# Kernel tuning notes

Hardware: AMD Instinct MI355X
Metric: run time of the kernel (lower is better)

Reference implementation:

```python
import jax, jax.numpy as jnp
import numpy as np

B, S, D = 4, 4096, 1024
E, C, F = 8, 1024, 2048


def setup_inputs() -> dict:
    key = jax.random.key(0)
    ks = jax.random.split(key, 6)
    # weight init per module: uniform(-bound, bound), bound = sqrt(3)*sqrt(1/3)/sqrt(fan_in) = 1/sqrt(fan_in)
    b_d = 1.0 / np.sqrt(D)
    b_f = 1.0 / np.sqrt(F)
    return {
        "x": jax.random.normal(ks[0], (B, S, D), dtype=jnp.float32),
        "expert_weights": jax.random.uniform(ks[1], (B, E, C), dtype=jnp.float32),
        "token_indices": jax.random.randint(ks[2], (B, E, C), 0, S, dtype=jnp.int64),
        "w1": jax.random.uniform(ks[3], (E, D, F), dtype=jnp.float32, minval=-b_d, maxval=b_d),
        "w2": jax.random.uniform(ks[4], (E, D, F), dtype=jnp.float32, minval=-b_d, maxval=b_d),
        "w3": jax.random.uniform(ks[5], (E, F, D), dtype=jnp.float32, minval=-b_f, maxval=b_f),
    }


def reference(x, expert_weights, token_indices, w1, w2, w3):
    # gather: each expert picks `capacity` tokens from its batch row
    b_idx = jnp.arange(B)[:, None, None]                      # (B,1,1)
    expert_inputs = x[b_idx, token_indices]                   # (B,E,C,D)
    # grouped swiglu FFN per expert (no weight repeat needed: einsum batches over E)
    gate = jax.nn.silu(jnp.einsum('becd,edf->becf', expert_inputs, w1))
    value = jnp.einsum('becd,edf->becf', expert_inputs, w2)
    expert_outputs = jnp.einsum('becf,efd->becd', gate * value, w3)  # (B,E,C,D)
    weighted = expert_outputs * expert_weights[..., None]     # (B,E,C,D)
    # weighted scatter-add combine back to (B,S,D)
    out = jnp.zeros((B, S, D), dtype=x.dtype)
    out = out.at[b_idx, token_indices].add(weighted)
    return out
```

## Files before the change

### kernel.cpp

```cpp
#include <hip/hip_runtime.h>

#define Bn 4
#define Sn 4096
#define Dn 1024
#define En 8
#define Cn 1024
#define Fn 2048
#define Mn (Bn * Cn)

typedef __bf16 bf16x4 __attribute__((ext_vector_type(4)));
typedef __bf16 bf16x8 __attribute__((ext_vector_type(8)));
typedef float f32x4 __attribute__((ext_vector_type(4)));

#define GLOAD16(gsrc, ldst)                                                    \
  __builtin_amdgcn_global_load_lds(                                            \
      (const __attribute__((address_space(1))) void*)(gsrc),                   \
      (__attribute__((address_space(3))) void*)(ldst), 16, 0, 0)

#define VMCNT3() asm volatile("s_waitcnt vmcnt(3)" ::: "memory")
#define VMCNT0() asm volatile("s_waitcnt vmcnt(0)" ::: "memory")
#define SCHEDB() __builtin_amdgcn_sched_barrier(0)
#define SBAR() __builtin_amdgcn_s_barrier()
#define PRIO(p) __builtin_amdgcn_s_setprio(p)

__global__ __launch_bounds__(256) void tcast_kernel(
    const float* __restrict__ in, __bf16* __restrict__ out, int K, int N) {
  __shared__ float t[32][33];
  const int e = blockIdx.z;
  const float* src = in + (size_t)e * K * N;
  __bf16* dst = out + (size_t)e * K * N;
  const int n0 = blockIdx.x << 5, k0 = blockIdx.y << 5;
  const int tx = threadIdx.x & 31, ty = threadIdx.x >> 5;
#pragma unroll
  for (int i = 0; i < 4; ++i)
    t[ty + i * 8][tx] = src[(size_t)(k0 + ty + i * 8) * N + (n0 + tx)];
  __syncthreads();
#pragma unroll
  for (int i = 0; i < 4; ++i)
    dst[(size_t)(n0 + ty + i * 8) * K + (k0 + tx)] = (__bf16)t[tx][ty + i * 8];
}

__global__ __launch_bounds__(256) void gather_cast_kernel(
    const float* __restrict__ x, const int* __restrict__ tok,
    __bf16* __restrict__ Xg) {
  const int gid = blockIdx.x * 4 + (threadIdx.x >> 6);
  const int lane = threadIdx.x & 63;
  const int e = gid >> 12, m = gid & 4095, b = m >> 10, c = m & 1023;
  const int t = tok[((size_t)b * En + e) * Cn + c];
  const float* src = x + ((size_t)b * Sn + t) * Dn;
  __bf16* dst = Xg + (size_t)gid * Dn;
#pragma unroll
  for (int i = 0; i < 4; ++i) {
    f32x4 v = *(const f32x4*)(src + i * 256 + lane * 4);
    bf16x4 o;
    o[0] = (__bf16)v[0];
    o[1] = (__bf16)v[1];
    o[2] = (__bf16)v[2];
    o[3] = (__bf16)v[3];
    *(bf16x4*)(dst + i * 256 + lane * 4) = o;
  }
}


__global__ __launch_bounds__(512, 4) void gemm12_kernel(
    const __bf16* __restrict__ Xg, const float* __restrict__ ew,
    const __bf16* __restrict__ w1T, const __bf16* __restrict__ w2T,
    __bf16* __restrict__ Hbh, int e0) {
  __shared__ __align__(16) char lds[73728];

  const int tid = threadIdx.x;
  const int lane = tid & 63, wid = tid >> 6;
  const int wr = wid >> 2, wc = wid & 3;
  const int mt = blockIdx.x, ft = blockIdx.y, eLoc = blockIdx.z;
  const int e = e0 + eLoc;

  const int srow = tid >> 2;
  const int sof = ((tid & 3) ^ ((tid >> 3) & 3)) << 3;
  const __bf16* pA = Xg + ((size_t)e * Mn + mt * 128 + srow) * Dn + sof;
  const __bf16* pB1 = w1T + ((size_t)e * Fn + ft * 128 + srow) * Dn + sof;
  const __bf16* pB2 = w2T + ((size_t)e * Fn + ft * 128 + srow) * Dn + sof;

  auto stage = [&](int slot) {
    char* d = lds + slot * 24576 + tid * 16;
    GLOAD16(pA, d);
    GLOAD16(pB1, d + 8192);
    GLOAD16(pB2, d + 16384);
    pA += 32;
    pB1 += 32;
    pB2 += 32;
  };

  const int rl = lane & 15, kb = lane >> 4;
  const int swz = (kb ^ ((rl >> 1) & 3)) << 4;

  f32x4 acc[4][4];
  const f32x4 z4 = {0.f, 0.f, 0.f, 0.f};
#pragma unroll
  for (int i = 0; i < 4; ++i)
#pragma unroll
    for (int j = 0; j < 4; ++j) acc[i][j] = z4;

  stage(0);
  stage(1);

  const int KT = Dn / 32;
#pragma unroll 1
  for (int c = 0; c < KT; ++c) {
    if (c < KT - 1) VMCNT3();
    else VMCNT0();
    SBAR();
    SCHEDB();
    const char* Ab = lds + (c % 3) * 24576;
    const char* Bb = Ab + 8192;
    bf16x8 a4[4], b4[4];
#pragma unroll
    for (int f = 0; f < 4; ++f) {
      const int ra = wr * 64 + f * 16 + rl;
      a4[f] = *(const bf16x8*)(Ab + ra * 64 + swz);
      const int rb = wc * 64 + f * 16 + rl;
      b4[f] = *(const bf16x8*)(Bb + rb * 64 + swz);
    }
    if (c + 2 < KT) stage((c + 2) % 3);
    PRIO(1);
#pragma unroll
    for (int fm = 0; fm < 4; ++fm)
#pragma unroll
      for (int fn = 0; fn < 4; ++fn)
        acc[fm][fn] = __builtin_amdgcn_mfma_f32_16x16x32_bf16(
            a4[fm], b4[fn], acc[fm][fn], 0, 0, 0);
    PRIO(0);
  }
  __syncthreads();

  const int rl0 = (lane >> 4) << 2, cl = lane & 15;
  if (wc >= 2) {
    char* reg = lds + (wr * 2 + (wc - 2)) * 8192;
#pragma unroll
    for (int fm = 0; fm < 4; ++fm)
#pragma unroll
      for (int fn = 0; fn < 4; ++fn)
#pragma unroll
        for (int j = 0; j < 4; ++j) {
          const int row = fm * 16 + rl0 + j;
          *(__bf16*)(reg + row * 128 + ((fn ^ ((row >> 2) & 3)) << 5) +
                     cl * 2) = (__bf16)acc[fm][fn][j];
        }
  }
  __syncthreads();
  if (wc < 2) {
    char* reg = lds + (wr * 2 + wc) * 8192;
    const int m0 = mt * 128 + wr * 64;
    const int b = m0 >> 10;
    const size_t ewBase = ((size_t)b * En + e) * Cn;
#pragma unroll
    for (int fm = 0; fm < 4; ++fm)
#pragma unroll
      for (int j = 0; j < 4; ++j) {
        const int row = fm * 16 + rl0 + j;
        const float wgt = ew[ewBase + ((m0 + row) & (Cn - 1))];
#pragma unroll
        for (int fn = 0; fn < 4; ++fn) {
          __bf16* p = (__bf16*)(reg + row * 128 +
                                ((fn ^ ((row >> 2) & 3)) << 5) + cl * 2);
          const float v = (float)*p;
          const float g = acc[fm][fn][j];
          *p = (__bf16)((g / (1.f + __expf(-g))) * v * wgt);
        }
      }
  }
  __syncthreads();
  __bf16* hBase = Hbh + ((size_t)eLoc * Mn + mt * 128) * Fn + ft * 128;
#pragma unroll
  for (int p = 0; p < 4; ++p) {
    const int row = p * 32 + (tid >> 4);
    const int c8 = (tid & 15) * 8;
    const int reg = (row >> 6) * 2 + (c8 >> 6);
    const int rr = row & 63, cc = c8 & 63;
    bf16x8 v = *(const bf16x8*)(lds + reg * 8192 + rr * 128 +
                                (((cc >> 4) ^ ((rr >> 2) & 3)) << 5) +
                                (cc & 15) * 2);
    *(bf16x8*)(hBase + (size_t)row * Fn + c8) = v;
  }
}

__global__ __launch_bounds__(512, 4) void gemm3_kernel(
    const __bf16* __restrict__ Hbh, const __bf16* __restrict__ w3T,
    const int* __restrict__ tok, float* __restrict__ out, int e0) {
  __shared__ __align__(16) char lds[73728];

  const int tid = threadIdx.x;
  const int lane = tid & 63, wid = tid >> 6;
  const int wr = wid >> 2, wc = wid & 3;
  const int mt = blockIdx.x, nt = blockIdx.y, eLoc = blockIdx.z;
  const int e = e0 + eLoc;

  const int srow = tid >> 2;
  const int sof = ((tid & 3) ^ ((tid >> 3) & 3)) << 3;
  const __bf16* pA = Hbh + ((size_t)eLoc * Mn + mt * 128 + srow) * Fn + sof;
  const __bf16* pB0 = w3T + ((size_t)e * Dn + nt * 256 + srow) * Fn + sof;
  const __bf16* pB1 = pB0 + (size_t)128 * Fn;

  auto stage = [&](int slot) {
    char* d = lds + slot * 24576 + tid * 16;
    GLOAD16(pA, d);
    GLOAD16(pB0, d + 8192);
    GLOAD16(pB1, d + 16384);
    pA += 32;
    pB0 += 32;
    pB1 += 32;
  };

  const int rl = lane & 15, kb = lane >> 4;
  const int swz = (kb ^ ((rl >> 1) & 3)) << 4;

  f32x4 acc[4][4];
  const f32x4 z4 = {0.f, 0.f, 0.f, 0.f};
#pragma unroll
  for (int i = 0; i < 4; ++i)
#pragma unroll
    for (int j = 0; j < 4; ++j) acc[i][j] = z4;

  stage(0);
  stage(1);

  const int KT = Fn / 32;
#pragma unroll 1
  for (int c = 0; c < KT; ++c) {
    if (c < KT - 1) VMCNT3();
    else VMCNT0();
    SBAR();
    SCHEDB();
    const char* Ab = lds + (c % 3) * 24576;
    const char* Bb = Ab + 8192;
    bf16x8 a4[4], b4[4];
#pragma unroll
    for (int f = 0; f < 4; ++f) {
      const int ra = wr * 64 + f * 16 + rl;
      a4[f] = *(const bf16x8*)(Ab + ra * 64 + swz);
      const int rb = wc * 64 + f * 16 + rl;
      b4[f] = *(const bf16x8*)(Bb + rb * 64 + swz);
    }
    if (c + 2 < KT) stage((c + 2) % 3);
    PRIO(1);
#pragma unroll
    for (int fm = 0; fm < 4; ++fm)
#pragma unroll
      for (int fn = 0; fn < 4; ++fn)
        acc[fm][fn] = __builtin_amdgcn_mfma_f32_16x16x32_bf16(
            a4[fm], b4[fn], acc[fm][fn], 0, 0, 0);
    PRIO(0);
  }

  const int m0 = mt * 128 + wr * 64;
  const int b = m0 >> 10;
  const int rl0 = (lane >> 4) << 2, cl = lane & 15;
  const int colBase = nt * 256 + wc * 64 + cl;
#pragma unroll
  for (int fm = 0; fm < 4; ++fm) {
#pragma unroll
    for (int j = 0; j < 4; ++j) {
      const int m = m0 + fm * 16 + rl0 + j;
      const int c2 = m & (Cn - 1);
      const int t = tok[((size_t)b * En + e) * Cn + c2];
      float* orow = out + ((size_t)b * Sn + t) * Dn + colBase;
#pragma unroll
      for (int fn = 0; fn < 4; ++fn)
        atomicAdd(orow + fn * 16, acc[fm][fn][j]);
    }
  }
}

extern "C" void kernel_launch(void* const* d_in, const int* in_sizes, int n_in,
                              void* d_out, int out_size, void* d_ws,
                              size_t ws_size, hipStream_t stream) {
  const float* x = (const float*)d_in[0];
  const float* ew = (const float*)d_in[1];
  const int* tok = (const int*)d_in[2];
  const float* w1 = (const float*)d_in[3];
  const float* w2 = (const float*)d_in[4];
  const float* w3 = (const float*)d_in[5];
  float* out = (float*)d_out;

  const size_t wE = (size_t)En * Dn * Fn;
  const size_t xgE = (size_t)En * Mn * Dn;
  const size_t hbE = (size_t)(En / 2) * Mn * Fn;
  __bf16* w1T = (__bf16*)d_ws;
  __bf16* w2T = w1T + wE;
  __bf16* w3T = w2T + wE;
  __bf16* Xg = w3T + wE;
  __bf16* Hbh = Xg + xgE;
  const size_t need = (3 * wE + xgE + hbE) * sizeof(__bf16);
  if (ws_size < need) return;

  (void)hipMemsetAsync(d_out, 0, (size_t)Bn * Sn * Dn * sizeof(float), stream);

  tcast_kernel<<<dim3(Fn / 32, Dn / 32, En), 256, 0, stream>>>(w1, w1T, Dn, Fn);
  tcast_kernel<<<dim3(Fn / 32, Dn / 32, En), 256, 0, stream>>>(w2, w2T, Dn, Fn);
  tcast_kernel<<<dim3(Dn / 32, Fn / 32, En), 256, 0, stream>>>(w3, w3T, Fn, Dn);
  gather_cast_kernel<<<dim3(En * Mn / 4), 256, 0, stream>>>(x, tok, Xg);
  for (int h = 0; h < 2; ++h) {
    gemm12_kernel<<<dim3(32, 16, En / 2), 512, 0, stream>>>(Xg, ew, w1T, w2T,
                                                            Hbh, h * (En / 2));
    gemm3_kernel<<<dim3(32, 4, En / 2), 512, 0, stream>>>(Hbh, w3T, tok, out,
                                                          h * (En / 2));
  }
}
```

Before: 653.6 us.

## Enlarge GEMM block tile to 256 rows with 1024-thread blocks

Both GEMM kernels move from 512-thread blocks with 128-row M tiles to 1024-thread blocks with 256-row M tiles. Each thread now issues two global-to-LDS loads per stage instead of three, so the wait count drops to vmcnt(2), and the LDS staging buffers grow to 96KB. The goal is better reuse of the staged weight tiles and fewer global loads per output. The cost is fewer blocks per expert group, larger LDS use that limits residency to one block per CU, and a 128-VGPR-per-thread cap that may cause spills.

```diff
diff --git a/kernel.cpp b/kernel.cpp
--- a/kernel.cpp
+++ b/kernel.cpp
@@ -17,7 +17,7 @@
       (const __attribute__((address_space(1))) void*)(gsrc),                   \
       (__attribute__((address_space(3))) void*)(ldst), 16, 0, 0)
 
-#define VMCNT3() asm volatile("s_waitcnt vmcnt(3)" ::: "memory")
+#define VMCNT2() asm volatile("s_waitcnt vmcnt(2)" ::: "memory")
 #define VMCNT0() asm volatile("s_waitcnt vmcnt(0)" ::: "memory")
 #define SCHEDB() __builtin_amdgcn_sched_barrier(0)
 #define SBAR() __builtin_amdgcn_s_barrier()
@@ -62,11 +62,11 @@
 }
 
 
-__global__ __launch_bounds__(512, 4) void gemm12_kernel(
+__global__ __launch_bounds__(1024, 4) void gemm12_kernel(
     const __bf16* __restrict__ Xg, const float* __restrict__ ew,
     const __bf16* __restrict__ w1T, const __bf16* __restrict__ w2T,
     __bf16* __restrict__ Hbh, int e0) {
-  __shared__ __align__(16) char lds[73728];
+  __shared__ __align__(16) char lds[98304];
 
   const int tid = threadIdx.x;
   const int lane = tid & 63, wid = tid >> 6;
@@ -76,18 +76,18 @@
 
   const int srow = tid >> 2;
   const int sof = ((tid & 3) ^ ((tid >> 3) & 3)) << 3;
-  const __bf16* pA = Xg + ((size_t)e * Mn + mt * 128 + srow) * Dn + sof;
-  const __bf16* pB1 = w1T + ((size_t)e * Fn + ft * 128 + srow) * Dn + sof;
-  const __bf16* pB2 = w2T + ((size_t)e * Fn + ft * 128 + srow) * Dn + sof;
+  const __bf16* pA = Xg + ((size_t)e * Mn + mt * 256 + srow) * Dn + sof;
+  const __bf16* pB =
+      (srow < 128)
+          ? w1T + ((size_t)e * Fn + ft * 128 + srow) * Dn + sof
+          : w2T + ((size_t)e * Fn + ft * 128 + (srow - 128)) * Dn + sof;
 
   auto stage = [&](int slot) {
-    char* d = lds + slot * 24576 + tid * 16;
+    char* d = lds + slot * 32768 + tid * 16;
     GLOAD16(pA, d);
-    GLOAD16(pB1, d + 8192);
-    GLOAD16(pB2, d + 16384);
+    GLOAD16(pB, d + 16384);
     pA += 32;
-    pB1 += 32;
-    pB2 += 32;
+    pB += 32;
   };
 
   const int rl = lane & 15, kb = lane >> 4;
@@ -106,12 +106,12 @@
   const int KT = Dn / 32;
 #pragma unroll 1
   for (int c = 0; c < KT; ++c) {
-    if (c < KT - 1) VMCNT3();
+    if (c < KT - 1) VMCNT2();
     else VMCNT0();
     SBAR();
     SCHEDB();
-    const char* Ab = lds + (c % 3) * 24576;
-    const char* Bb = Ab + 8192;
+    const char* Ab = lds + (c % 3) * 32768;
+    const char* Bb = Ab + 16384;
     bf16x8 a4[4], b4[4];
 #pragma unroll
     for (int f = 0; f < 4; ++f) {
@@ -149,7 +149,7 @@
   __syncthreads();
   if (wc < 2) {
     char* reg = lds + (wr * 2 + wc) * 8192;
-    const int m0 = mt * 128 + wr * 64;
+    const int m0 = mt * 256 + wr * 64;
     const int b = m0 >> 10;
     const size_t ewBase = ((size_t)b * En + e) * Cn;
 #pragma unroll
@@ -169,24 +169,24 @@
       }
   }
   __syncthreads();
-  __bf16* hBase = Hbh + ((size_t)eLoc * Mn + mt * 128) * Fn + ft * 128;
+  __bf16* hBase = Hbh + ((size_t)eLoc * Mn + mt * 256) * Fn + ft * 128;
 #pragma unroll
   for (int p = 0; p < 4; ++p) {
-    const int row = p * 32 + (tid >> 4);
+    const int row = p * 64 + (tid >> 4);
     const int c8 = (tid & 15) * 8;
-    const int reg = (row >> 6) * 2 + (c8 >> 6);
+    const int region = ((row >> 6) << 1) + (c8 >> 6);
     const int rr = row & 63, cc = c8 & 63;
-    bf16x8 v = *(const bf16x8*)(lds + reg * 8192 + rr * 128 +
+    bf16x8 v = *(const bf16x8*)(lds + region * 8192 + rr * 128 +
                                 (((cc >> 4) ^ ((rr >> 2) & 3)) << 5) +
                                 (cc & 15) * 2);
     *(bf16x8*)(hBase + (size_t)row * Fn + c8) = v;
   }
 }
 
-__global__ __launch_bounds__(512, 4) void gemm3_kernel(
+__global__ __launch_bounds__(1024, 4) void gemm3_kernel(
     const __bf16* __restrict__ Hbh, const __bf16* __restrict__ w3T,
     const int* __restrict__ tok, float* __restrict__ out, int e0) {
-  __shared__ __align__(16) char lds[73728];
+  __shared__ __align__(16) char lds[98304];
 
   const int tid = threadIdx.x;
   const int lane = tid & 63, wid = tid >> 6;
@@ -196,18 +196,15 @@
 
   const int srow = tid >> 2;
   const int sof = ((tid & 3) ^ ((tid >> 3) & 3)) << 3;
-  const __bf16* pA = Hbh + ((size_t)eLoc * Mn + mt * 128 + srow) * Fn + sof;
-  const __bf16* pB0 = w3T + ((size_t)e * Dn + nt * 256 + srow) * Fn + sof;
-  const __bf16* pB1 = pB0 + (size_t)128 * Fn;
+  const __bf16* pA = Hbh + ((size_t)eLoc * Mn + mt * 256 + srow) * Fn + sof;
+  const __bf16* pB = w3T + ((size_t)e * Dn + nt * 256 + srow) * Fn + sof;
 
   auto stage = [&](int slot) {
-    char* d = lds + slot * 24576 + tid * 16;
+    char* d = lds + slot * 32768 + tid * 16;
     GLOAD16(pA, d);
-    GLOAD16(pB0, d + 8192);
-    GLOAD16(pB1, d + 16384);
+    GLOAD16(pB, d + 16384);
     pA += 32;
-    pB0 += 32;
-    pB1 += 32;
+    pB += 32;
   };
 
   const int rl = lane & 15, kb = lane >> 4;
@@ -226,12 +223,12 @@
   const int KT = Fn / 32;
 #pragma unroll 1
   for (int c = 0; c < KT; ++c) {
-    if (c < KT - 1) VMCNT3();
+    if (c < KT - 1) VMCNT2();
     else VMCNT0();
     SBAR();
     SCHEDB();
-    const char* Ab = lds + (c % 3) * 24576;
-    const char* Bb = Ab + 8192;
+    const char* Ab = lds + (c % 3) * 32768;
+    const char* Bb = Ab + 16384;
     bf16x8 a4[4], b4[4];
 #pragma unroll
     for (int f = 0; f < 4; ++f) {
@@ -251,7 +248,7 @@
     PRIO(0);
   }
 
-  const int m0 = mt * 128 + wr * 64;
+  const int m0 = mt * 256 + wr * 64;
   const int b = m0 >> 10;
   const int rl0 = (lane >> 4) << 2, cl = lane & 15;
   const int colBase = nt * 256 + wc * 64 + cl;
@@ -299,9 +296,9 @@
   tcast_kernel<<<dim3(Dn / 32, Fn / 32, En), 256, 0, stream>>>(w3, w3T, Fn, Dn);
   gather_cast_kernel<<<dim3(En * Mn / 4), 256, 0, stream>>>(x, tok, Xg);
   for (int h = 0; h < 2; ++h) {
-    gemm12_kernel<<<dim3(32, 16, En / 2), 512, 0, stream>>>(Xg, ew, w1T, w2T,
-                                                            Hbh, h * (En / 2));
-    gemm3_kernel<<<dim3(32, 4, En / 2), 512, 0, stream>>>(Hbh, w3T, tok, out,
-                                                          h * (En / 2));
-  }
-}
+    gemm12_kernel<<<dim3(16, 16, En / 2), 1024, 0, stream>>>(Xg, ew, w1T, w2T,
+                                                             Hbh, h * (En / 2));
+    gemm3_kernel<<<dim3(16, 4, En / 2), 1024, 0, stream>>>(Hbh, w3T, tok, out,
+                                                           h * (En / 2));
+  }
+}
```

New measurement: 654.2 us. Within noise of the previous version (+0.1%).
